# Optimization experiments

Hardware: AMD Instinct MI355X
Metric: run time of the kernel (lower is better)

Reference implementation:

```python
import jax, jax.numpy as jnp
import numpy as np

D = 1024
H = 16
DH = D // H
L = 128  # max_pos_len
B = 4
T = 1024
SCALE = float(np.sqrt(D / H))


def setup_inputs() -> dict:
    key = jax.random.key(0)
    ks = jax.random.split(key, 9)
    x_q = jax.random.normal(ks[0], (B, T, D), dtype=jnp.float32)
    x_k = jax.random.normal(ks[1], (B, T, D), dtype=jnp.float32)
    x_v = jax.random.normal(ks[2], (B, T, D), dtype=jnp.float32)
    mask = jax.random.randint(ks[3], (B, 1, 1, T), 0, 2) == 1  # bool, True = masked
    Wq = jax.random.normal(ks[4], (D, D), dtype=jnp.float32) * 0.02
    Wk = jax.random.normal(ks[5], (D, D), dtype=jnp.float32) * 0.02
    Wv = jax.random.normal(ks[6], (D, D), dtype=jnp.float32) * 0.02
    Wo = jax.random.normal(ks[7], (D, D), dtype=jnp.float32) * 0.02
    pos_emb = jax.random.normal(ks[8], (2 * L + 1, DH), dtype=jnp.float32)
    return {"x_q": x_q, "x_k": x_k, "x_v": x_v, "mask": mask,
            "Wq": Wq, "Wk": Wk, "Wv": Wv, "Wo": Wo, "pos_emb": pos_emb}


def reference(x_q, x_k, x_v, mask, Wq, Wk, Wv, Wo, pos_emb):
    # nn.Linear(bias=False): y = x @ W.T
    def split_heads(x):  # (B,T,D) -> (B,H,T,DH)
        return x.reshape(B, -1, H, DH).transpose(0, 2, 1, 3)

    Q = split_heads(x_q @ Wq.T)
    K = split_heads(x_k @ Wk.T)
    V = split_heads(x_v @ Wv.T)

    logits = jnp.einsum('bhqd,bhkd->bhqk', Q, K)

    # arrange_char_pos_embedding: indices[q,k] = clamp(k-q, -L, L) + L
    rel = jnp.clip(jnp.arange(T)[None, :] - jnp.arange(T)[:, None], -L, L) + L
    arranged_pos = pos_emb[rel]  # (T_Q, T_K, DH)
    pos_logits = jnp.einsum('bhqd,qkd->bhqk', Q, arranged_pos)

    logits = (logits + pos_logits) / SCALE
    logits = jnp.where(mask, -jnp.inf, logits)  # mask broadcasts (B,1,1,T)
    attn = jax.nn.softmax(logits, axis=-1)  # dropout p=0.0 -> identity

    combined = jnp.einsum('bhqk,bhkd->bhqd', attn, V)
    heads_concat = combined.transpose(0, 2, 1, 3).reshape(B, -1, D)
    return heads_concat @ Wo.T
```

## Files before the change

### kernel.cpp

```cpp
#include <hip/hip_runtime.h>
#include <hip/hip_bf16.h>
#include <stdint.h>

typedef __attribute__((ext_vector_type(8))) short short8;
typedef __attribute__((ext_vector_type(4))) float f32x4;

__device__ __forceinline__ uint16_t f2bf(float f) {
    union { float f; uint32_t u; } v; v.f = f;
    uint32_t r = v.u + 0x7FFF + ((v.u >> 16) & 1);
    return (uint16_t)(r >> 16);
}
__device__ __forceinline__ float bf2f(uint16_t u) {
    union { uint32_t u; float f; } v; v.u = ((uint32_t)u) << 16;
    return v.f;
}
__device__ __forceinline__ float exp2_raw(float x) {
    float r;
    asm("v_exp_f32 %0, %1" : "=v"(r) : "v"(x));
    return r;
}
__device__ __forceinline__ uint32_t cvt_pk_bf16(float lo, float hi) {
    uint32_t r;
    asm("v_cvt_pk_bf16_f32 %0, %1, %2" : "=v"(r) : "v"(lo), "v"(hi));
    return r;
}

template<int F32>
__device__ __forceinline__ uint4 load8(const void* p, size_t off) {
    if (F32) {
        const float* f = (const float*)p + off;
        float4 f0 = *(const float4*)f;
        float4 f1 = *(const float4*)(f + 4);
        uint4 r;
        r.x = (uint32_t)f2bf(f0.x) | ((uint32_t)f2bf(f0.y) << 16);
        r.y = (uint32_t)f2bf(f0.z) | ((uint32_t)f2bf(f0.w) << 16);
        r.z = (uint32_t)f2bf(f1.x) | ((uint32_t)f2bf(f1.y) << 16);
        r.w = (uint32_t)f2bf(f1.z) | ((uint32_t)f2bf(f1.w) << 16);
        return r;
    } else {
        return *(const uint4*)((const uint16_t*)p + off);
    }
}

#define GLDS(gp, lp) __builtin_amdgcn_global_load_lds( \
    (const __attribute__((address_space(1))) void*)(gp), \
    (__attribute__((address_space(3))) void*)(lp), 16, 0, 0)

struct CvtSeg { const float* s; uint16_t* d; int n8; };
struct CvtArgs {
    CvtSeg seg[9]; int nseg;
    const void* mraw; unsigned long long* mbits; uint16_t* mvals;
};

__global__ __launch_bounds__(256) void cvt_bf16(CvtArgs a)
{
    if (blockIdx.x == 0) {
        __shared__ int flags[3];
        __shared__ uint8_t mloc[4096];
        const uint32_t* w = (const uint32_t*)a.mraw;
        const uint8_t* b8 = (const uint8_t*)a.mraw;
        const int t = threadIdx.x;
        if (t < 3) flags[t] = 0;
        __syncthreads();
        int fbyte = 0, ff32 = 0, fodd = 0;
        for (int i = t; i < 1024; i += 256) {
            uint32_t v = w[i];
            if (v != 0u && v != 1u && v != 0x3F800000u) fbyte = 1;
            if (v == 0x3F800000u) ff32 = 1;
            if ((i & 1) && v != 0u) fodd = 1;
        }
        if (fbyte) atomicOr(&flags[0], 1);
        if (ff32)  atomicOr(&flags[1], 1);
        if (fodd)  atomicOr(&flags[2], 1);
        __syncthreads();
        int mode;
        if (flags[0]) mode = 1;
        else if (flags[1]) mode = 0;
        else if (!flags[2]) mode = 2;
        else mode = 0;
        for (int k = t; k < 4096; k += 256) {
            int val;
            if (mode == 1)      val = (b8[k] != 0);
            else if (mode == 2) val = (w[2 * k] != 0u);
            else                val = (w[k] != 0u);
            mloc[k] = (uint8_t)val;
        }
        __syncthreads();
        for (int k = t; k < 4096; k += 256)
            a.mvals[k] = mloc[k] ? (uint16_t)0 : (uint16_t)0x3F80;
        if (t < 64) {
            uint64_t bits = 0;
#pragma unroll
            for (int i = 0; i < 64; ++i)
                bits |= (uint64_t)mloc[t * 64 + i] << i;
            a.mbits[t] = bits;
        }
    }
    const int tid = blockIdx.x * 256 + threadIdx.x;
    const int stride = gridDim.x * 256;
    for (int s = 0; s < a.nseg; ++s) {
        const float* src = a.seg[s].s;
        uint16_t* dst = a.seg[s].d;
        const int n8 = a.seg[s].n8;
        if (src) {
            for (int i = tid; i < n8; i += stride)
                *(uint4*)(dst + (size_t)i * 8) = load8<1>(src, (size_t)i * 8);
        } else {
            const uint4 z = {0u, 0u, 0u, 0u};
            for (int i = tid; i < n8; i += stride)
                *(uint4*)(dst + (size_t)i * 8) = z;
        }
    }
}

__global__ __launch_bounds__(256) void gemm128_qkv(
    const uint16_t* __restrict__ xq, const uint16_t* __restrict__ xk, const uint16_t* __restrict__ xv,
    const uint16_t* __restrict__ Wq, const uint16_t* __restrict__ Wk, const uint16_t* __restrict__ Wv,
    uint16_t* __restrict__ Qh, uint16_t* __restrict__ Khd, uint16_t* __restrict__ Vt,
    const unsigned long long* __restrict__ mbits)
{
    __shared__ alignas(16) uint16_t As[2][128 * 32];
    __shared__ alignas(16) uint16_t Bs[2][128 * 32];

    const int z = blockIdx.z;
    const uint16_t* A = (z == 0) ? xq : (z == 1) ? xk : xv;
    const uint16_t* B = (z == 0) ? Wq : (z == 1) ? Wk : Wv;
    uint16_t* C = (z == 0) ? Qh : (z == 1) ? Khd : Vt;
    const int cm = (z == 2) ? 2 : 1;
    const int bm = blockIdx.x, bn = blockIdx.y;
    const int K = 1024;

    const int t = threadIdx.x;
    const int lane = t & 63, wave = t >> 6;
    const int lrow = lane & 15, quad = lane >> 4;
    const int wr = (wave >> 1) * 64, wc = (wave & 1) * 64;
    const int g_row = wave * 16 + (lane >> 2);
    const int g_col = (lane & 3) * 8;

    const f32x4 fz = {0.f, 0.f, 0.f, 0.f};
    f32x4 acc[4][4];
#pragma unroll
    for (int i = 0; i < 4; ++i)
#pragma unroll
        for (int j = 0; j < 4; ++j) acc[i][j] = fz;

    for (int k0 = 0; k0 < K; k0 += 64) {
        __syncthreads();
#pragma unroll
        for (int kh = 0; kh < 2; ++kh) {
            const int kk = k0 + kh * 32;
            GLDS(A + (size_t)(bm * 128 + g_row) * K + kk + g_col,      As[kh] + wave * 512);
            GLDS(A + (size_t)(bm * 128 + g_row + 64) * K + kk + g_col, As[kh] + wave * 512 + 2048);
            GLDS(B + (size_t)(bn * 128 + g_row) * K + kk + g_col,      Bs[kh] + wave * 512);
            GLDS(B + (size_t)(bn * 128 + g_row + 64) * K + kk + g_col, Bs[kh] + wave * 512 + 2048);
        }
        __syncthreads();

#pragma unroll
        for (int kh = 0; kh < 2; ++kh) {
            short8 a[4], b[4];
#pragma unroll
            for (int i = 0; i < 4; ++i)
                a[i] = *(const short8*)(As[kh] + (wr + i * 16 + lrow) * 32 + quad * 8);
#pragma unroll
            for (int j = 0; j < 4; ++j)
                b[j] = *(const short8*)(Bs[kh] + (wc + j * 16 + lrow) * 32 + quad * 8);
#pragma unroll
            for (int i = 0; i < 4; ++i)
#pragma unroll
                for (int j = 0; j < 4; ++j)
                    acc[i][j] = __builtin_amdgcn_mfma_f32_16x16x32_bf16(a[i], b[j], acc[i][j], 0, 0, 0);
        }
    }

    if (cm == 2) {
        __syncthreads();
        uint16_t* scr = As[0] + wave * 1024;
        const int mg0 = bm * 128 + wr;
        const int widx = __builtin_amdgcn_readfirstlane((mg0 >> 10) * 16 + ((mg0 & 1023) >> 6));
        const uint64_t mword = mbits[widx];
        const uint64_t mw64 = mword >> ((lane & 1) * 8);
#pragma unroll
        for (int i = 0; i < 4; ++i)
#pragma unroll
            for (int j = 0; j < 4; ++j) {
                uint2 pk;
                pk.x = (uint32_t)f2bf(acc[i][j][0]) | ((uint32_t)f2bf(acc[i][j][1]) << 16);
                pk.y = (uint32_t)f2bf(acc[i][j][2]) | ((uint32_t)f2bf(acc[i][j][3]) << 16);
                *(uint2*)(scr + lrow * 16 + quad * 4) = pk;
                if (lane < 32) {
                    int n = lane >> 1, m8 = (lane & 1) * 8;
                    short8 vv = *(const short8*)(scr + n * 16 + m8);
                    int ng = bn * 128 + wc + j * 16 + n;
                    int hh = ng >> 6, d = ng & 63;
                    int mg = bm * 128 + wr + i * 16;
                    int bb = mg >> 10, tl = (mg & 1023) + m8;
                    uint32_t eb = (uint32_t)(mw64 >> (i * 16)) & 0xFFu;
                    if (eb) {
                        union { short8 s; uint32_t u[4]; } uw;
                        uw.s = vv;
#pragma unroll
                        for (int c = 0; c < 4; ++c) {
                            uint32_t km = (((eb >> (2 * c)) & 1) ? 0u : 0x0000FFFFu)
                                        | (((eb >> (2 * c + 1)) & 1) ? 0u : 0xFFFF0000u);
                            uw.u[c] &= km;
                        }
                        vv = uw.s;
                    }
                    size_t addr = (size_t)(bb * 16 + hh) * 65536
                                + (size_t)((tl >> 6) * 4096
                                           + ((d >> 4) * 2 + ((tl >> 5) & 1)) * 512
                                           + ((tl >> 3) & 3) * 128 + (d & 15) * 8);
                    *(short8*)(C + addr) = vv;
                }
            }
        return;
    }

#pragma unroll
    for (int i = 0; i < 4; ++i)
#pragma unroll
        for (int j = 0; j < 4; ++j)
#pragma unroll
            for (int r = 0; r < 4; ++r) {
                int m = bm * 128 + wr + i * 16 + quad * 4 + r;
                int n = bn * 128 + wc + j * 16 + lrow;
                int bb = m >> 10, key = m & 1023, hh = n >> 6, d = n & 63;
                if (z == 0) {
                    C[(((size_t)bb * 16 + hh) * 1024 + key) * 64 + d] = f2bf(acc[i][j][r]);
                } else {
                    size_t addr = (size_t)(bb * 16 + hh) * 65536
                                + (size_t)((key >> 6) * 4096
                                           + (((key >> 4) & 3) * 2 + (d >> 5)) * 512
                                           + ((d >> 3) & 3) * 128 + (key & 15) * 8 + (d & 7));
                    C[addr] = f2bf(acc[i][j][r]);
                }
            }
}

__global__ __launch_bounds__(256) void gemm_out(
    const uint16_t* __restrict__ A, const uint16_t* __restrict__ B,
    float* __restrict__ C, int M, int N, int K)
{
    __shared__ alignas(16) uint16_t As[2][64 * 32];
    __shared__ alignas(16) uint16_t Bs[2][128 * 32];

    const int t = threadIdx.x;
    const int lane = t & 63, wave = t >> 6;
    const int lrow = lane & 15, quad = lane >> 4;
    const int wr = (wave >> 1) * 32, wc = (wave & 1) * 64;
    const int g_row = wave * 16 + (lane >> 2);
    const int g_col = (lane & 3) * 8;
    const int bm = blockIdx.x, bn = blockIdx.y;

    const f32x4 fz = {0.f, 0.f, 0.f, 0.f};
    f32x4 acc[2][4];
#pragma unroll
    for (int i = 0; i < 2; ++i)
#pragma unroll
        for (int j = 0; j < 4; ++j) acc[i][j] = fz;

    for (int k0 = 0; k0 < K; k0 += 64) {
        __syncthreads();
#pragma unroll
        for (int kh = 0; kh < 2; ++kh) {
            const int kk = k0 + kh * 32;
            GLDS(A + (size_t)(bm * 64 + g_row) * K + kk + g_col,       As[kh] + wave * 512);
            GLDS(B + (size_t)(bn * 128 + g_row) * K + kk + g_col,      Bs[kh] + wave * 512);
            GLDS(B + (size_t)(bn * 128 + g_row + 64) * K + kk + g_col, Bs[kh] + wave * 512 + 2048);
        }
        __syncthreads();

#pragma unroll
        for (int kh = 0; kh < 2; ++kh) {
            short8 a[2], b[4];
#pragma unroll
            for (int i = 0; i < 2; ++i)
                a[i] = *(const short8*)(As[kh] + (wr + i * 16 + lrow) * 32 + quad * 8);
#pragma unroll
            for (int j = 0; j < 4; ++j)
                b[j] = *(const short8*)(Bs[kh] + (wc + j * 16 + lrow) * 32 + quad * 8);
#pragma unroll
            for (int i = 0; i < 2; ++i)
#pragma unroll
                for (int j = 0; j < 4; ++j)
                    acc[i][j] = __builtin_amdgcn_mfma_f32_16x16x32_bf16(a[i], b[j], acc[i][j], 0, 0, 0);
        }
    }

#pragma unroll
    for (int i = 0; i < 2; ++i)
#pragma unroll
        for (int j = 0; j < 4; ++j)
#pragma unroll
            for (int r = 0; r < 4; ++r) {
                int m = bm * 64 + wr + i * 16 + quad * 4 + r;
                int n = bn * 128 + wc + j * 16 + lrow;
                C[(size_t)m * N + n] = acc[i][j][r];
            }
}

#define FA_SM(KB_)                                                              \
{                                                                               \
    const int diff = (KB_) - qb;                                                \
    if (diff <= -192 || diff >= 144) {                                          \
        const bool low = (diff <= -192);                                        \
        _Pragma("unroll")                                                       \
        for (int j = 0; j < 4; ++j) {                                           \
            float e[4];                                                         \
            _Pragma("unroll")                                                   \
            for (int r = 0; r < 4; ++r) {                                       \
                float pc = low ? pcl[r] : pch[r];                               \
                e[r] = exp2_raw(__builtin_fmaf(s[j][r], CS, pc));               \
            }                                                                   \
            const uint32_t p01 = cvt_pk_bf16(e[0], e[1]);                       \
            const uint32_t p23 = cvt_pk_bf16(e[2], e[3]);                       \
            const int col = j * 16 + lrow;                                      \
            const int rw = quad * 4;                                            \
            Pl[wave][rw + 0][col] = (uint16_t)p01;                              \
            Pl[wave][rw + 1][col] = (uint16_t)(p01 >> 16);                      \
            Pl[wave][rw + 2][col] = (uint16_t)p23;                              \
            Pl[wave][rw + 3][col] = (uint16_t)(p23 >> 16);                      \
        }                                                                       \
    } else {                                                                    \
        _Pragma("unroll")                                                       \
        for (int j = 0; j < 4; ++j) {                                           \
            const int key = (KB_) + j * 16 + lrow;                              \
            float e[4];                                                         \
            _Pragma("unroll")                                                   \
            for (int r = 0; r < 4; ++r) {                                       \
                int q = qb + quad * 4 + r;                                      \
                int ql = q & 63;                                                \
                int rel = min(max(key - q, -128), 128) + 128;                   \
                float p = bf2f(Qpos_l[ql][rel]);                                \
                e[r] = exp2_raw(__builtin_fmaf(s[j][r], CS, p));                \
            }                                                                   \
            const uint32_t p01 = cvt_pk_bf16(e[0], e[1]);                       \
            const uint32_t p23 = cvt_pk_bf16(e[2], e[3]);                       \
            const int col = j * 16 + lrow;                                      \
            const int rw = quad * 4;                                            \
            Pl[wave][rw + 0][col] = (uint16_t)p01;                              \
            Pl[wave][rw + 1][col] = (uint16_t)(p01 >> 16);                      \
            Pl[wave][rw + 2][col] = (uint16_t)p23;                              \
            Pl[wave][rw + 3][col] = (uint16_t)(p23 >> 16);                      \
        }                                                                       \
    }                                                                           \
    ap0 = *(const short8*)(&Pl[wave][lrow][quad * 8]);                          \
    ap1 = *(const short8*)(&Pl[wave][lrow][32 + quad * 8]);                     \
}

#define FA_BODY(TI, KC, KN, MC, MN)                                             \
{                                                                               \
    const int kb = (TI) * 64;                                                   \
                      \
    const uint16_t* vb = Vp + (size_t)(TI) * 4096;                              \
    short8 vv[8];                                                               \
    _Pragma("unroll")                                                           \
    for (int sl = 0; sl < 8; ++sl)                                              \
        vv[sl] = *(const short8*)(vb + sl * 512 + lane8);                       \
                                               \
    const int tn = ((TI) + 1) & 15;                                             \
    const uint16_t* kbn = Kp + (size_t)tn * 4096;                               \
    _Pragma("unroll")                                                           \
    for (int sl = 0; sl < 8; ++sl)                                              \
        KN[sl] = *(const short8*)(kbn + sl * 512 + lane8);                      \
    MN[0] = *(const short8*)(mkb + tn * 64 + quad * 8);                         \
    MN[1] = *(const short8*)(mkb + tn * 64 + 32 + quad * 8);                    \
    f32x4 s[4];                                                                 \
    __builtin_amdgcn_s_setprio(1);                                              \
    _Pragma("unroll")                                                           \
    for (int j = 0; j < 4; ++j) {                                               \
        s[j] = __builtin_amdgcn_mfma_f32_16x16x32_bf16(aq0, KC[j * 2 + 0], fz, 0, 0, 0); \
        s[j] = __builtin_amdgcn_mfma_f32_16x16x32_bf16(aq1, KC[j * 2 + 1], s[j], 0, 0, 0); \
    }                                                                           \
    __builtin_amdgcn_s_setprio(0);                                              \
    FA_SM(kb)                                                                   \
    __builtin_amdgcn_s_setprio(1);                                              \
    _Pragma("unroll")                                                           \
    for (int dt = 0; dt < 4; ++dt) {                                            \
        o[dt] = __builtin_amdgcn_mfma_f32_16x16x32_bf16(ap0, vv[dt * 2 + 0], o[dt], 0, 0, 0); \
        o[dt] = __builtin_amdgcn_mfma_f32_16x16x32_bf16(ap1, vv[dt * 2 + 1], o[dt], 0, 0, 0); \
    }                                                                           \
    lacc = __builtin_amdgcn_mfma_f32_16x16x32_bf16(ap0, MC[0], lacc, 0, 0, 0);  \
    lacc = __builtin_amdgcn_mfma_f32_16x16x32_bf16(ap1, MC[1], lacc, 0, 0, 0);  \
    __builtin_amdgcn_s_setprio(0);                                              \
}

__global__ __launch_bounds__(256) void flash_attn(
    const uint16_t* __restrict__ Qh, const uint16_t* __restrict__ Kh,
    const uint16_t* __restrict__ Vt, const uint16_t* __restrict__ pos,
    const uint16_t* __restrict__ maskv, uint16_t* __restrict__ comb)
{
    const int blk = blockIdx.x;
    const int jj = blk >> 3;
    const int bh = (blk & 7) * 8 + (jj >> 4);
    const int qt = jj & 15;
    const int b = bh >> 4;
    const int h = bh & 15;
    const int t = threadIdx.x;
    const int lane = t & 63;
    const int wave = t >> 6;
    const int lrow = lane & 15;
    const int quad = lane >> 4;
    const int qb = qt * 64 + wave * 16;
    const int lane8 = lane * 8;

    __shared__ alignas(16) uint16_t Qpos_l[64][277];
    __shared__ alignas(16) uint16_t Pl[4][16][72];

    const uint16_t* Kp = Kh + (size_t)bh * 65536;
    const uint16_t* Vp = Vt + (size_t)bh * 65536;
    const uint16_t* mkb = maskv + (size_t)b * 1024;

    const float CS = 0.18033688011f;

    short8 ka[8], kn[8], ma[2], mn[2];
#pragma unroll
    for (int sl = 0; sl < 8; ++sl)
        ka[sl] = *(const short8*)(Kp + sl * 512 + lane8);
    ma[0] = *(const short8*)(mkb + quad * 8);
    ma[1] = *(const short8*)(mkb + 32 + quad * 8);

    const uint16_t* Qp = Qh + ((size_t)bh * 1024 + qb) * 64;
    short8 aq0 = *(const short8*)(Qp + (size_t)lrow * 64 + quad * 8);
    short8 aq1 = *(const short8*)(Qp + (size_t)lrow * 64 + 32 + quad * 8);

    const f32x4 fz = {0.f, 0.f, 0.f, 0.f};

#pragma unroll 4
    for (int nt = 0; nt < 17; ++nt) {
        short8 pb0 = *(const short8*)(pos + (size_t)(nt * 16 + lrow) * 64 + quad * 8);
        short8 pb1 = *(const short8*)(pos + (size_t)(nt * 16 + lrow) * 64 + 32 + quad * 8);
        f32x4 c = __builtin_amdgcn_mfma_f32_16x16x32_bf16(aq0, pb0, fz, 0, 0, 0);
        c = __builtin_amdgcn_mfma_f32_16x16x32_bf16(aq1, pb1, c, 0, 0, 0);
        const uint32_t p01 = cvt_pk_bf16(c[0] * CS, c[1] * CS);
        const uint32_t p23 = cvt_pk_bf16(c[2] * CS, c[3] * CS);
        const int row = wave * 16 + quad * 4;
        const int col = nt * 16 + lrow;
        Qpos_l[row + 0][col] = (uint16_t)p01;
        Qpos_l[row + 1][col] = (uint16_t)(p01 >> 16);
        Qpos_l[row + 2][col] = (uint16_t)p23;
        Qpos_l[row + 3][col] = (uint16_t)(p23 >> 16);
    }

    float pcl[4], pch[4];
#pragma unroll
    for (int r = 0; r < 4; ++r) {
        int ql = wave * 16 + quad * 4 + r;
        pcl[r] = bf2f(Qpos_l[ql][0]);
        pch[r] = bf2f(Qpos_l[ql][256]);
    }

    f32x4 o[4] = {fz, fz, fz, fz};
    f32x4 lacc = fz;
    short8 ap0, ap1;

    for (int t2 = 0; t2 < 16; t2 += 2) {
        FA_BODY(t2, ka, kn, ma, mn)
        FA_BODY(t2 + 1, kn, ka, mn, ma)
    }

    float inv[4];
#pragma unroll
    for (int r = 0; r < 4; ++r) inv[r] = 1.0f / lacc[r];

#pragma unroll
    for (int dt = 0; dt < 4; ++dt)
#pragma unroll
        for (int r = 0; r < 4; ++r) {
            size_t row = (size_t)b * 1024 + qb + quad * 4 + r;
            size_t col = (size_t)h * 64 + dt * 16 + lrow;
            comb[row * 1024 + col] = f2bf(o[dt][r] * inv[r]);
        }
}

extern "C" void kernel_launch(void* const* d_in, const int* in_sizes, int n_in,
                              void* d_out, int out_size, void* d_ws, size_t ws_size,
                              hipStream_t stream)
{
    const float* x_q = (const float*)d_in[0];
    const float* x_k = (const float*)d_in[1];
    const float* x_v = (const float*)d_in[2];
    const void*  msk = d_in[3];
    const float* Wq  = (const float*)d_in[4];
    const float* Wk  = (const float*)d_in[5];
    const float* Wv  = (const float*)d_in[6];
    const float* Wo  = (const float*)d_in[7];
    const float* pos = (const float*)d_in[8];

    char* ws = (char*)d_ws;
    const size_t MB = 1u << 20;
    uint16_t* Qh   = (uint16_t*)(ws);
    uint16_t* Khd  = (uint16_t*)(ws + 8 * MB);
    uint16_t* Vt   = (uint16_t*)(ws + 16 * MB);
    uint16_t* xqb  = (uint16_t*)(ws + 24 * MB);
    uint16_t* xkb  = (uint16_t*)(ws + 32 * MB);
    uint16_t* xvb  = (uint16_t*)(ws + 40 * MB);
    uint16_t* Wqb  = (uint16_t*)(ws + 48 * MB);
    uint16_t* Wkb  = (uint16_t*)(ws + 50 * MB);
    uint16_t* Wvb  = (uint16_t*)(ws + 52 * MB);
    uint16_t* Wob  = (uint16_t*)(ws + 54 * MB);
    uint16_t* posb = (uint16_t*)(ws + 56 * MB);
    unsigned long long* mbits = (unsigned long long*)(ws + 56 * MB + 65536);
    uint16_t* mvals = (uint16_t*)(ws + 56 * MB + 65536 + 4096);
    uint16_t* comb = xqb;

    CvtArgs ca{};
    int ns = 0;
    ca.seg[ns++] = {x_q, xqb, 524288};
    ca.seg[ns++] = {x_k, xkb, 524288};
    ca.seg[ns++] = {x_v, xvb, 524288};
    ca.seg[ns++] = {Wq, Wqb, 131072};
    ca.seg[ns++] = {Wk, Wkb, 131072};
    ca.seg[ns++] = {Wv, Wvb, 131072};
    ca.seg[ns++] = {Wo, Wob, 131072};
    ca.seg[ns++] = {pos, posb, 2056};
    ca.seg[ns++] = {nullptr, posb + 16448, 120};
    ca.nseg = ns;
    ca.mraw = msk;
    ca.mbits = mbits;
    ca.mvals = mvals;
    cvt_bf16<<<dim3(512), dim3(256), 0, stream>>>(ca);

    gemm128_qkv<<<dim3(32, 8, 3), dim3(256), 0, stream>>>(
        xqb, xkb, xvb, Wqb, Wkb, Wvb, Qh, Khd, Vt, mbits);

    flash_attn<<<dim3(1024), dim3(256), 0, stream>>>(Qh, Khd, Vt, posb, mvals, comb);

    gemm_out<<<dim3(64, 8), dim3(256), 0, stream>>>(
        comb, Wob, (float*)d_out, 4096, 1024, 1024);
}
```

Baseline: 245.5 us.

## Swizzle attention LDS tiles, compute pos-bias edge separately, add K pack kernel

The QKV GEMM epilogue now writes K in plain head-major layout, and a new kpack kernel rearranges it with 16-byte vector copies into the fragment-packed layout that flash attention reads. This replaces the scattered 2-byte stores in the GEMM epilogue. Inside flash attention, the padded Qpos and P shared-memory tiles become unpadded XOR-swizzled tiles to avoid bank conflicts while using less LDS. The rel=256 edge column is computed with a separate MFMA plus a shuffle instead of being stored in LDS, and launch bounds now request 4 blocks per CU. The cost is an extra kernel launch and an extra pass over K in global memory.

Result: slower. 413.4 us (+68.4%).

```diff
diff --git a/kernel.cpp b/kernel.cpp
--- a/kernel.cpp
+++ b/kernel.cpp
@@ -225,17 +225,24 @@
             for (int r = 0; r < 4; ++r) {
                 int m = bm * 128 + wr + i * 16 + quad * 4 + r;
                 int n = bn * 128 + wc + j * 16 + lrow;
-                int bb = m >> 10, key = m & 1023, hh = n >> 6, d = n & 63;
-                if (z == 0) {
-                    C[(((size_t)bb * 16 + hh) * 1024 + key) * 64 + d] = f2bf(acc[i][j][r]);
-                } else {
-                    size_t addr = (size_t)(bb * 16 + hh) * 65536
-                                + (size_t)((key >> 6) * 4096
-                                           + (((key >> 4) & 3) * 2 + (d >> 5)) * 512
-                                           + ((d >> 3) & 3) * 128 + (key & 15) * 8 + (d & 7));
-                    C[addr] = f2bf(acc[i][j][r]);
-                }
+                int bb = m >> 10, tt = m & 1023, hh = n >> 6, d = n & 63;
+                C[(((size_t)bb * 16 + hh) * 1024 + tt) * 64 + d] = f2bf(acc[i][j][r]);
             }
+}
+
+__global__ __launch_bounds__(256) void kpack(
+    const uint16_t* __restrict__ Kin, uint16_t* __restrict__ Kout)
+{
+    const int tid = blockIdx.x * 256 + threadIdx.x;
+    const int key = tid & 1023;
+    const int d0 = ((tid >> 10) & 7) * 8;
+    const int bh = tid >> 13;
+    short8 v = *(const short8*)(Kin + ((size_t)bh << 16) + key * 64 + d0);
+    size_t addr = ((size_t)bh << 16)
+                + (size_t)((key >> 6) * 4096
+                           + (((key >> 4) & 3) * 2 + (d0 >> 5)) * 512
+                           + ((d0 >> 3) & 3) * 128 + (key & 15) * 8);
+    *(short8*)(Kout + addr) = v;
 }
 
 __global__ __launch_bounds__(256) void gemm_out(
@@ -316,11 +323,11 @@
             const uint32_t p01 = cvt_pk_bf16(e[0], e[1]);                       \
             const uint32_t p23 = cvt_pk_bf16(e[2], e[3]);                       \
             const int col = j * 16 + lrow;                                      \
-            const int rw = quad * 4;                                            \
-            Pl[wave][rw + 0][col] = (uint16_t)p01;                              \
-            Pl[wave][rw + 1][col] = (uint16_t)(p01 >> 16);                      \
-            Pl[wave][rw + 2][col] = (uint16_t)p23;                              \
-            Pl[wave][rw + 3][col] = (uint16_t)(p23 >> 16);                      \
+            const int colb = col & 7, colh = col >> 3;                          \
+            Plw[(rw0 + 0) * 64 + ((colh ^ (x4 + 0)) << 3) + colb] = (uint16_t)p01;         \
+            Plw[(rw0 + 1) * 64 + ((colh ^ (x4 + 1)) << 3) + colb] = (uint16_t)(p01 >> 16); \
+            Plw[(rw0 + 2) * 64 + ((colh ^ (x4 + 2)) << 3) + colb] = (uint16_t)p23;         \
+            Plw[(rw0 + 3) * 64 + ((colh ^ (x4 + 3)) << 3) + colb] = (uint16_t)(p23 >> 16); \
         }                                                                       \
     } else {                                                                    \
         _Pragma("unroll")                                                       \
@@ -332,35 +339,34 @@
                 int q = qb + quad * 4 + r;                                      \
                 int ql = q & 63;                                                \
                 int rel = min(max(key - q, -128), 128) + 128;                   \
-                float p = bf2f(Qpos_l[ql][rel]);                                \
+                float p = (rel >= 256) ? pch[r]                                 \
+                        : bf2f(Qpos_l[ql][rel ^ q8]);                           \
                 e[r] = exp2_raw(__builtin_fmaf(s[j][r], CS, p));                \
             }                                                                   \
             const uint32_t p01 = cvt_pk_bf16(e[0], e[1]);                       \
             const uint32_t p23 = cvt_pk_bf16(e[2], e[3]);                       \
             const int col = j * 16 + lrow;                                      \
-            const int rw = quad * 4;                                            \
-            Pl[wave][rw + 0][col] = (uint16_t)p01;                              \
-            Pl[wave][rw + 1][col] = (uint16_t)(p01 >> 16);                      \
-            Pl[wave][rw + 2][col] = (uint16_t)p23;                              \
-            Pl[wave][rw + 3][col] = (uint16_t)(p23 >> 16);                      \
+            const int colb = col & 7, colh = col >> 3;                          \
+            Plw[(rw0 + 0) * 64 + ((colh ^ (x4 + 0)) << 3) + colb] = (uint16_t)p01;         \
+            Plw[(rw0 + 1) * 64 + ((colh ^ (x4 + 1)) << 3) + colb] = (uint16_t)(p01 >> 16); \
+            Plw[(rw0 + 2) * 64 + ((colh ^ (x4 + 2)) << 3) + colb] = (uint16_t)p23;         \
+            Plw[(rw0 + 3) * 64 + ((colh ^ (x4 + 3)) << 3) + colb] = (uint16_t)(p23 >> 16); \
         }                                                                       \
     }                                                                           \
-    ap0 = *(const short8*)(&Pl[wave][lrow][quad * 8]);                          \
-    ap1 = *(const short8*)(&Pl[wave][lrow][32 + quad * 8]);                     \
+    ap0 = *(const short8*)(Plw + lrow * 64 + ((quad ^ l7) << 3));               \
+    ap1 = *(const short8*)(Plw + lrow * 64 + (((quad + 4) ^ l7) << 3));         \
 }
 
 #define FA_BODY(TI, KC, KN, MC, MN)                                             \
 {                                                                               \
     const int kb = (TI) * 64;                                                   \
-                      \
     const uint16_t* vb = Vp + (size_t)(TI) * 4096;                              \
     short8 vv[8];                                                               \
     _Pragma("unroll")                                                           \
     for (int sl = 0; sl < 8; ++sl)                                              \
         vv[sl] = *(const short8*)(vb + sl * 512 + lane8);                       \
-                                               \
     const int tn = ((TI) + 1) & 15;                                             \
-    const uint16_t* kbn = Kp + (size_t)tn * 4096;                               \
+    const uint16_t* kbn = Kf + (size_t)tn * 4096;                               \
     _Pragma("unroll")                                                           \
     for (int sl = 0; sl < 8; ++sl)                                              \
         KN[sl] = *(const short8*)(kbn + sl * 512 + lane8);                      \
@@ -386,8 +392,8 @@
     __builtin_amdgcn_s_setprio(0);                                              \
 }
 
-__global__ __launch_bounds__(256) void flash_attn(
-    const uint16_t* __restrict__ Qh, const uint16_t* __restrict__ Kh,
+__global__ __launch_bounds__(256, 4) void flash_attn(
+    const uint16_t* __restrict__ Qh, const uint16_t* __restrict__ Kfg,
     const uint16_t* __restrict__ Vt, const uint16_t* __restrict__ pos,
     const uint16_t* __restrict__ maskv, uint16_t* __restrict__ comb)
 {
@@ -404,11 +410,16 @@
     const int quad = lane >> 4;
     const int qb = qt * 64 + wave * 16;
     const int lane8 = lane * 8;
-
-    __shared__ alignas(16) uint16_t Qpos_l[64][277];
-    __shared__ alignas(16) uint16_t Pl[4][16][72];
-
-    const uint16_t* Kp = Kh + (size_t)bh * 65536;
+    const int q8 = quad << 3;
+    const int l7 = lrow & 7;
+    const int rw0 = quad * 4;
+    const int x4 = (quad & 1) * 4;
+
+    __shared__ alignas(16) uint16_t Qpos_l[64][256];
+    __shared__ alignas(16) uint16_t Pl[4][1024];
+    uint16_t* Plw = Pl[wave];
+
+    const uint16_t* Kf = Kfg + (size_t)bh * 65536;
     const uint16_t* Vp = Vt + (size_t)bh * 65536;
     const uint16_t* mkb = maskv + (size_t)b * 1024;
 
@@ -417,7 +428,7 @@
     short8 ka[8], kn[8], ma[2], mn[2];
 #pragma unroll
     for (int sl = 0; sl < 8; ++sl)
-        ka[sl] = *(const short8*)(Kp + sl * 512 + lane8);
+        ka[sl] = *(const short8*)(Kf + sl * 512 + lane8);
     ma[0] = *(const short8*)(mkb + quad * 8);
     ma[1] = *(const short8*)(mkb + 32 + quad * 8);
 
@@ -428,27 +439,33 @@
     const f32x4 fz = {0.f, 0.f, 0.f, 0.f};
 
 #pragma unroll 4
-    for (int nt = 0; nt < 17; ++nt) {
+    for (int nt = 0; nt < 16; ++nt) {
         short8 pb0 = *(const short8*)(pos + (size_t)(nt * 16 + lrow) * 64 + quad * 8);
         short8 pb1 = *(const short8*)(pos + (size_t)(nt * 16 + lrow) * 64 + 32 + quad * 8);
         f32x4 c = __builtin_amdgcn_mfma_f32_16x16x32_bf16(aq0, pb0, fz, 0, 0, 0);
         c = __builtin_amdgcn_mfma_f32_16x16x32_bf16(aq1, pb1, c, 0, 0, 0);
         const uint32_t p01 = cvt_pk_bf16(c[0] * CS, c[1] * CS);
         const uint32_t p23 = cvt_pk_bf16(c[2] * CS, c[3] * CS);
-        const int row = wave * 16 + quad * 4;
-        const int col = nt * 16 + lrow;
-        Qpos_l[row + 0][col] = (uint16_t)p01;
-        Qpos_l[row + 1][col] = (uint16_t)(p01 >> 16);
-        Qpos_l[row + 2][col] = (uint16_t)p23;
-        Qpos_l[row + 3][col] = (uint16_t)(p23 >> 16);
+        const int row = wave * 16 + rw0;
+        const int colswz = (nt * 16 + lrow) ^ q8;
+        Qpos_l[row + 0][colswz] = (uint16_t)p01;
+        Qpos_l[row + 1][colswz] = (uint16_t)(p01 >> 16);
+        Qpos_l[row + 2][colswz] = (uint16_t)p23;
+        Qpos_l[row + 3][colswz] = (uint16_t)(p23 >> 16);
     }
 
     float pcl[4], pch[4];
-#pragma unroll
-    for (int r = 0; r < 4; ++r) {
-        int ql = wave * 16 + quad * 4 + r;
-        pcl[r] = bf2f(Qpos_l[ql][0]);
-        pch[r] = bf2f(Qpos_l[ql][256]);
+    {
+        short8 pb0 = *(const short8*)(pos + (size_t)(256 + lrow) * 64 + quad * 8);
+        short8 pb1 = *(const short8*)(pos + (size_t)(256 + lrow) * 64 + 32 + quad * 8);
+        f32x4 c = __builtin_amdgcn_mfma_f32_16x16x32_bf16(aq0, pb0, fz, 0, 0, 0);
+        c = __builtin_amdgcn_mfma_f32_16x16x32_bf16(aq1, pb1, c, 0, 0, 0);
+#pragma unroll
+        for (int r = 0; r < 4; ++r)
+            pch[r] = __shfl(c[r], lane & 48) * CS;
+#pragma unroll
+        for (int r = 0; r < 4; ++r)
+            pcl[r] = bf2f(Qpos_l[wave * 16 + rw0 + r][q8]);
     }
 
     f32x4 o[4] = {fz, fz, fz, fz};
@@ -503,6 +520,7 @@
     uint16_t* posb = (uint16_t*)(ws + 56 * MB);
     unsigned long long* mbits = (unsigned long long*)(ws + 56 * MB + 65536);
     uint16_t* mvals = (uint16_t*)(ws + 56 * MB + 65536 + 4096);
+    uint16_t* Kfg  = (uint16_t*)(ws + 57 * MB);
     uint16_t* comb = xqb;
 
     CvtArgs ca{};
@@ -525,7 +543,9 @@
     gemm128_qkv<<<dim3(32, 8, 3), dim3(256), 0, stream>>>(
         xqb, xkb, xvb, Wqb, Wkb, Wvb, Qh, Khd, Vt, mbits);
 
-    flash_attn<<<dim3(1024), dim3(256), 0, stream>>>(Qh, Khd, Vt, posb, mvals, comb);
+    kpack<<<dim3(2048), dim3(256), 0, stream>>>(Khd, Kfg);
+
+    flash_attn<<<dim3(1024), dim3(256), 0, stream>>>(Qh, Kfg, Vt, posb, mvals, comb);
 
     gemm_out<<<dim3(64, 8), dim3(256), 0, stream>>>(
         comb, Wob, (float*)d_out, 4096, 1024, 1024);
```
